# Optimization experiments

Measured on AMD Instinct MI355X. Metric: run time of the kernel, lower is better.

Reference implementation:

```python
import jax, jax.numpy as jnp
import numpy as np

NV, NC, NI = 20000, 300, 10000
NN = NV + NC + NI
E = 1_000_000
D = 64
HOPS = 2


def _segmax(src, idx, mask, n_seg):
    # scatter_max with torch_scatter semantics: empty segments -> 0
    idxm = jnp.where(mask, idx, n_seg)  # route masked edges to dump segment
    m = jax.ops.segment_max(src, idxm, num_segments=n_seg + 1)[:n_seg]
    return jnp.where(jnp.isfinite(m), m, 0.0)


def _segmin(src, idx, mask, n_seg):
    idxm = jnp.where(mask, idx, n_seg)
    m = jax.ops.segment_min(src, idxm, num_segments=n_seg + 1)[:n_seg]
    return jnp.where(jnp.isfinite(m), m, 0.0)


def _segmax_all(src, idx, n_seg):
    m = jax.ops.segment_max(src, idx, num_segments=n_seg)
    return jnp.where(jnp.isfinite(m), m, 0.0)


def _center(src, idx, mask, n_seg, W1, b1, W2, b2):
    # CenterIntersection: MLP -> scatter_softmax -> weighted scatter_sum
    idxm = jnp.where(mask, idx, n_seg)
    h = jax.nn.relu(src @ W1.T + b1)
    a = h @ W2.T + b2
    a = jnp.where(mask[:, None], a, 0.0)
    m = jax.ops.segment_max(a, idxm, num_segments=n_seg + 1)
    m = jnp.where(jnp.isfinite(m), m, 0.0)
    e = jnp.where(mask[:, None], jnp.exp(a - m[idxm]), 0.0)
    s = jax.ops.segment_sum(e, idxm, num_segments=n_seg + 1)
    att = e / jnp.where(s > 0, s, 1.0)[idxm]
    out = jax.ops.segment_sum(att * src, idxm, num_segments=n_seg + 1)
    return out[:n_seg]


def _l2norm(x, eps=1e-12):
    n = jnp.linalg.norm(x, axis=-1, keepdims=True)
    return x / jnp.maximum(n, eps)


def setup_inputs() -> dict:
    key = jax.random.key(0)
    ks = jax.random.split(key, 16)
    n = lambda k, s: jax.random.normal(k, s, dtype=jnp.float32)
    return dict(
        visit_emb=n(ks[0], (NV, D)), visit_offset=n(ks[1], (NV, D)),
        ccs_emb=n(ks[2], (NC, D)), ccs_offset=n(ks[3], (NC, D)),
        icd_emb=n(ks[4], (NI, D)), icd_offset=n(ks[5], (NI, D)),
        head=jax.random.randint(ks[6], (E,), 0, NN),
        tail=jax.random.randint(ks[7], (E,), 0, NN),
        visit_time=jax.random.uniform(ks[8], (NV,), minval=1.0, maxval=50.0, dtype=jnp.float32),
        cW1=n(ks[9], (D, D)) * 0.1, cb1=jnp.zeros((D,), jnp.float32),
        cW2=n(ks[10], (D, D)) * 0.1, cb2=jnp.zeros((D,), jnp.float32),
        tW1=n(ks[11], (1, 1)), tb1=jnp.zeros((1,), jnp.float32),
        tW2=n(ks[12], (1, 1)), tb2=jnp.zeros((1,), jnp.float32),
    )


def reference(visit_emb, visit_offset, ccs_emb, ccs_offset, icd_emb, icd_offset,
              head, tail, visit_time, cW1, cb1, cW2, cb2, tW1, tb1, tW2, tb2):
    all_embs = jnp.concatenate([visit_emb, ccs_emb, icd_emb], axis=0)          # [NN, D]
    all_off = jax.nn.relu(jnp.concatenate([visit_offset, ccs_offset, icd_offset], axis=0))

    # time attention: [NV, 1]
    t = (1.0 / visit_time)[:, None]
    l1 = jax.nn.relu(t @ tW1.T + tb1)
    time_emb = jax.nn.softmax(l1 @ tW2.T + tb2, axis=0)

    hv = head < NV
    uidx = jnp.tile(jnp.arange(NV), 3)

    for _ in range(HOPS):
        ev = hv & (tail >= NV)
        vv = hv & (tail < NV)
        # center aggregation: entity->visit hop, then time-weighted visit->visit hop
        hist = all_embs[tail]                                                  # [E, D]
        agg1 = _center(hist, head, ev, NN, cW1, cb1, cW2, cb2)
        agg2 = agg1[:NV] * time_emb
        hist2 = agg2[jnp.where(vv, tail, 0)]
        agg = _center(hist2, head, vv, NN, cW1, cb1, cW2, cb2)

        # box offset aggregation per edge type
        off_t = jax.nn.relu(all_off[tail])                                     # [E, D]
        iv = hv & (tail >= NV) & (tail < NV + NC)
        vi = hv & (tail >= NV + NC)
        iv_off = _segmax(off_t, head, iv, NN)[:NV]
        ut_off = _segmax(off_t, head, vi, NN)[:NV]
        vv_off = _segmax(off_t, head, vv, NN)[:NV]
        visit_off = jax.nn.relu(
            _segmax_all(jnp.concatenate([iv_off, ut_off, vv_off], axis=0), uidx, NV))
        cm = (head >= NV) & (head < NV + NC)
        ccs_off = _segmax(off_t, head, cm, NN)[NV:NV + NC]
        im = head >= NV + NC
        icd_off = _segmin(off_t, head, im, NN)[NV + NC:]

        all_embs = _l2norm(agg)
        all_off = jax.nn.relu(jnp.concatenate([visit_off, ccs_off, icd_off], axis=0))

    return all_embs[:NV], all_off[:NV]
```

## Files before the change

### kernel.cpp

```cpp
#include <hip/hip_runtime.h>

#define NV 20000
#define NC 300
#define NI 10000
#define NN 30300
#define NE 1000000
#define D  64

#define NB     128
#define BNODES 237
#define CAP    12288
#define BIN_CHUNK 2048
#define NBLK_BIN ((NE + BIN_CHUNK - 1) / BIN_CHUNK)

__device__ __forceinline__ unsigned short f2bf(float x) {
    unsigned u = __float_as_uint(x);
    u += 0x7FFFu + ((u >> 16) & 1u);
    return (unsigned short)(u >> 16);
}

__global__ void init_off_kernel(const float4* __restrict__ vo, const float4* __restrict__ co,
                                const float4* __restrict__ io, unsigned short* __restrict__ buf,
                                float4* __restrict__ outz) {
    int i = blockIdx.x * blockDim.x + threadIdx.x;
    if (i >= NN * 16) return;
    if (i < NV * 16) outz[i] = make_float4(0.f, 0.f, 0.f, 0.f);
    int n = i >> 4;
    float4 v;
    if (n < NV)            v = vo[i];
    else if (n < NV + NC)  v = co[i - NV * 16];
    else                   v = io[i - (NV + NC) * 16];
    ushort4 o;
    o.x = f2bf(fmaxf(v.x, 0.f));
    o.y = f2bf(fmaxf(v.y, 0.f));
    o.z = f2bf(fmaxf(v.z, 0.f));
    o.w = f2bf(fmaxf(v.w, 0.f));
    *reinterpret_cast<ushort4*>(buf + (size_t)i * 4) = o;
}

__global__ void bin_kernel(const int* __restrict__ head, const int* __restrict__ tail,
                           int* __restrict__ gcur, unsigned* __restrict__ pairs) {
    __shared__ int hist[NB];
    __shared__ int base[NB];
    int t = threadIdx.x;
    int e0 = blockIdx.x * BIN_CHUNK;
    if (t < NB) hist[t] = 0;
    __syncthreads();
    int hs[8], ts[8];
    if (e0 + BIN_CHUNK <= NE) {
        const int4* h4 = reinterpret_cast<const int4*>(head + e0);
        const int4* t4 = reinterpret_cast<const int4*>(tail + e0);
        int4 ha = h4[t], hb = h4[256 + t];
        int4 ta = t4[t], tb = t4[256 + t];
        hs[0] = ha.x; hs[1] = ha.y; hs[2] = ha.z; hs[3] = ha.w;
        hs[4] = hb.x; hs[5] = hb.y; hs[6] = hb.z; hs[7] = hb.w;
        ts[0] = ta.x; ts[1] = ta.y; ts[2] = ta.z; ts[3] = ta.w;
        ts[4] = tb.x; ts[5] = tb.y; ts[6] = tb.z; ts[7] = tb.w;
#pragma unroll
        for (int i = 0; i < 8; i++) atomicAdd(&hist[hs[i] / BNODES], 1);
    } else {
#pragma unroll
        for (int i = 0; i < 8; i++) {
            int e = e0 + i * 256 + t;
            if (e < NE) {
                hs[i] = head[e]; ts[i] = tail[e];
                atomicAdd(&hist[hs[i] / BNODES], 1);
            } else hs[i] = -1;
        }
    }
    __syncthreads();
    if (t < NB) {
        int c = hist[t];
        base[t] = c ? atomicAdd(&gcur[t], c) : 0;
        hist[t] = 0;
    }
    __syncthreads();
#pragma unroll
    for (int i = 0; i < 8; i++) {
        if (hs[i] >= 0) {
            int b = hs[i] / BNODES;
            int pos = base[b] + atomicAdd(&hist[b], 1);
            if (pos < CAP)
                pairs[(size_t)b * CAP + pos] = ((unsigned)hs[i] << 15) | (unsigned)ts[i];
        }
    }
}

__global__ void bucket_sort_kernel(const unsigned* __restrict__ pairs, const int* __restrict__ gcur,
                                   unsigned short* __restrict__ stails,
                                   int* __restrict__ starts, int* __restrict__ ends) {
    __shared__ unsigned short staging[CAP];
    __shared__ int cnt_l[256];
    __shared__ int scan_s[256];
    __shared__ int cur[256];
    int b = blockIdx.x, t = threadIdx.x;
    int node0 = b * BNODES;
    int nn = min(BNODES, NN - node0);
    int cnt = min(gcur[b], CAP);
    cnt_l[t] = 0;
    __syncthreads();
    const unsigned* P = pairs + (size_t)b * CAP;
    for (int i = t; i < cnt; i += 256) {
        int local = (int)(P[i] >> 15) - node0;
        atomicAdd(&cnt_l[local], 1);
    }
    __syncthreads();
    int v = cnt_l[t];
    scan_s[t] = v;
    __syncthreads();
    for (int off = 1; off < 256; off <<= 1) {
        int tv = (t >= off) ? scan_s[t - off] : 0;
        __syncthreads();
        scan_s[t] += tv;
        __syncthreads();
    }
    int excl = scan_s[t] - v;
    cur[t] = excl;
    if (t < nn) {
        starts[node0 + t] = b * CAP + excl;
        ends[node0 + t]   = b * CAP + excl + v;
    }
    __syncthreads();
    for (int i = t; i < cnt; i += 256) {
        unsigned p = P[i];
        int local = (int)(p >> 15) - node0;
        int pos = atomicAdd(&cur[local], 1);
        staging[pos] = (unsigned short)(p & 0x7FFFu);
    }
    __syncthreads();
    for (int i = t; i < cnt; i += 256)
        stails[(size_t)b * CAP + i] = staging[i];
}

template<bool F32OUT>
__global__ __launch_bounds__(256) void hop_kernel(
        const unsigned short* __restrict__ prev,
        const int* __restrict__ starts, const int* __restrict__ ends,
        const unsigned short* __restrict__ stails,
        void* __restrict__ outp, int nNodes) {
    int wid  = blockIdx.x * 4 + (threadIdx.x >> 6);
    int lane = threadIdx.x & 63;
    if (wid >= nNodes) return;
    int start = starts[wid], end = ends[wid];
    bool isMin = (!F32OUT) && (wid >= NV + NC);
    unsigned mm = isMin ? 0xFFFFFFFFu : 0u;
    int grp = lane >> 4, sub = lane & 15;
    const unsigned short* rowb = prev + sub * 4;
    unsigned a0 = 0, a1 = 0, a2 = 0, a3 = 0;
    int k = start;
    for (; k + 16 <= end; k += 16) {
#pragma unroll
        for (int r = 0; r < 4; ++r) {
            int tix = (int)stails[k + r * 4 + grp];
            uint2 v = *reinterpret_cast<const uint2*>(rowb + tix * D);
            v.x ^= mm; v.y ^= mm;
            a0 = max(a0, v.x & 0xFFFFu); a1 = max(a1, v.x >> 16);
            a2 = max(a2, v.y & 0xFFFFu); a3 = max(a3, v.y >> 16);
        }
    }
    for (; k < end; k += 4) {
        int e = k + grp;
        int tix = (int)stails[(e < end) ? e : (end - 1)];
        uint2 v = *reinterpret_cast<const uint2*>(rowb + tix * D);
        if (e >= end) { v.x = mm; v.y = mm; }
        v.x ^= mm; v.y ^= mm;
        a0 = max(a0, v.x & 0xFFFFu); a1 = max(a1, v.x >> 16);
        a2 = max(a2, v.y & 0xFFFFu); a3 = max(a3, v.y >> 16);
    }
    a0 = max(a0, (unsigned)__shfl_xor((int)a0, 16)); a0 = max(a0, (unsigned)__shfl_xor((int)a0, 32));
    a1 = max(a1, (unsigned)__shfl_xor((int)a1, 16)); a1 = max(a1, (unsigned)__shfl_xor((int)a1, 32));
    a2 = max(a2, (unsigned)__shfl_xor((int)a2, 16)); a2 = max(a2, (unsigned)__shfl_xor((int)a2, 32));
    a3 = max(a3, (unsigned)__shfl_xor((int)a3, 16)); a3 = max(a3, (unsigned)__shfl_xor((int)a3, 32));
    unsigned m16 = mm & 0xFFFFu;
    unsigned r0 = a0 ^ m16, r1 = a1 ^ m16, r2 = a2 ^ m16, r3 = a3 ^ m16;
    if (start >= end) { r0 = r1 = r2 = r3 = 0; }
    if (grp == 0) {
        if (F32OUT) {
            float4 o = make_float4(__uint_as_float(r0 << 16), __uint_as_float(r1 << 16),
                                   __uint_as_float(r2 << 16), __uint_as_float(r3 << 16));
            reinterpret_cast<float4*>(outp)[(size_t)wid * 16 + sub] = o;
        } else {
            ushort4 o;
            o.x = (unsigned short)r0; o.y = (unsigned short)r1;
            o.z = (unsigned short)r2; o.w = (unsigned short)r3;
            reinterpret_cast<ushort4*>(outp)[(size_t)wid * 16 + sub] = o;
        }
    }
}

extern "C" void kernel_launch(void* const* d_in, const int* in_sizes, int n_in,
                              void* d_out, int out_size, void* d_ws, size_t ws_size,
                              hipStream_t stream) {
    const float* visit_offset = (const float*)d_in[1];
    const float* ccs_offset   = (const float*)d_in[3];
    const float* icd_offset   = (const float*)d_in[5];
    const int*   head         = (const int*)d_in[6];
    const int*   tail         = (const int*)d_in[7];
    float*       out          = (float*)d_out;

    char* ws = (char*)d_ws;
    unsigned short* off0   = (unsigned short*)(ws);
    unsigned short* off1   = (unsigned short*)(ws + (4u << 20));
    unsigned*       pairs  = (unsigned*)      (ws + (8u << 20));
    unsigned short* stails = (unsigned short*)(ws + (14u << 20));
    int*            starts = (int*)           (ws + (17u << 20));
    int*            ends   = (int*)           (ws + (17u << 20) + (256u << 10));
    int*            gcur   = (int*)           (ws + (17u << 20) + (512u << 10));

    hipMemsetAsync(gcur, 0, NB * sizeof(int), stream);

    init_off_kernel<<<(NN * 16 + 255) / 256, 256, 0, stream>>>(
        (const float4*)visit_offset, (const float4*)ccs_offset, (const float4*)icd_offset,
        off0, (float4*)out);
    bin_kernel<<<NBLK_BIN, 256, 0, stream>>>(head, tail, gcur, pairs);
    bucket_sort_kernel<<<NB, 256, 0, stream>>>(pairs, gcur, stails, starts, ends);

    hop_kernel<false><<<(NN + 3) / 4, 256, 0, stream>>>(off0, starts, ends, stails, off1, NN);
    hop_kernel<true><<<(NV + 3) / 4, 256, 0, stream>>>(off1, starts, ends, stails,
                                                       out + (size_t)NV * D, NV);
}
```

Before: 163.6 us.

## Use finer node buckets, 16-byte gathers with shuffled tails, fold counter reset

Result: faster. 153.3 us (-6.3%).

```diff
diff --git a/kernel.cpp b/kernel.cpp
--- a/kernel.cpp
+++ b/kernel.cpp
@@ -7,9 +7,9 @@
 #define NE 1000000
 #define D  64
 
-#define NB     128
-#define BNODES 237
-#define CAP    12288
+#define NB     512
+#define BNODES 60
+#define CAP    2560
 #define BIN_CHUNK 2048
 #define NBLK_BIN ((NE + BIN_CHUNK - 1) / BIN_CHUNK)
 
@@ -21,8 +21,12 @@
 
 __global__ void init_off_kernel(const float4* __restrict__ vo, const float4* __restrict__ co,
                                 const float4* __restrict__ io, unsigned short* __restrict__ buf,
-                                float4* __restrict__ outz) {
+                                float4* __restrict__ outz, int* __restrict__ gcur) {
     int i = blockIdx.x * blockDim.x + threadIdx.x;
+    if (blockIdx.x == 0) {
+        gcur[threadIdx.x] = 0;
+        gcur[threadIdx.x + 256] = 0;
+    }
     if (i >= NN * 16) return;
     if (i < NV * 16) outz[i] = make_float4(0.f, 0.f, 0.f, 0.f);
     int n = i >> 4;
@@ -44,7 +48,7 @@
     __shared__ int base[NB];
     int t = threadIdx.x;
     int e0 = blockIdx.x * BIN_CHUNK;
-    if (t < NB) hist[t] = 0;
+    for (int j = t; j < NB; j += 256) hist[j] = 0;
     __syncthreads();
     int hs[8], ts[8];
     if (e0 + BIN_CHUNK <= NE) {
@@ -69,10 +73,10 @@
         }
     }
     __syncthreads();
-    if (t < NB) {
-        int c = hist[t];
-        base[t] = c ? atomicAdd(&gcur[t], c) : 0;
-        hist[t] = 0;
+    for (int j = t; j < NB; j += 256) {
+        int c = hist[j];
+        base[j] = c ? atomicAdd(&gcur[j], c) : 0;
+        hist[j] = 0;
     }
     __syncthreads();
 #pragma unroll
@@ -144,46 +148,58 @@
     int start = starts[wid], end = ends[wid];
     bool isMin = (!F32OUT) && (wid >= NV + NC);
     unsigned mm = isMin ? 0xFFFFFFFFu : 0u;
-    int grp = lane >> 4, sub = lane & 15;
-    const unsigned short* rowb = prev + sub * 4;
-    unsigned a0 = 0, a1 = 0, a2 = 0, a3 = 0;
-    int k = start;
-    for (; k + 16 <= end; k += 16) {
-#pragma unroll
-        for (int r = 0; r < 4; ++r) {
-            int tix = (int)stails[k + r * 4 + grp];
-            uint2 v = *reinterpret_cast<const uint2*>(rowb + tix * D);
-            v.x ^= mm; v.y ^= mm;
-            a0 = max(a0, v.x & 0xFFFFu); a1 = max(a1, v.x >> 16);
-            a2 = max(a2, v.y & 0xFFFFu); a3 = max(a3, v.y >> 16);
-        }
-    }
-    for (; k < end; k += 4) {
-        int e = k + grp;
-        int tix = (int)stails[(e < end) ? e : (end - 1)];
-        uint2 v = *reinterpret_cast<const uint2*>(rowb + tix * D);
-        if (e >= end) { v.x = mm; v.y = mm; }
-        v.x ^= mm; v.y ^= mm;
-        a0 = max(a0, v.x & 0xFFFFu); a1 = max(a1, v.x >> 16);
-        a2 = max(a2, v.y & 0xFFFFu); a3 = max(a3, v.y >> 16);
-    }
-    a0 = max(a0, (unsigned)__shfl_xor((int)a0, 16)); a0 = max(a0, (unsigned)__shfl_xor((int)a0, 32));
-    a1 = max(a1, (unsigned)__shfl_xor((int)a1, 16)); a1 = max(a1, (unsigned)__shfl_xor((int)a1, 32));
-    a2 = max(a2, (unsigned)__shfl_xor((int)a2, 16)); a2 = max(a2, (unsigned)__shfl_xor((int)a2, 32));
-    a3 = max(a3, (unsigned)__shfl_xor((int)a3, 16)); a3 = max(a3, (unsigned)__shfl_xor((int)a3, 32));
+    int grp = lane >> 3, sub = lane & 7;
+    const unsigned short* rowb = prev + sub * 8;
+    unsigned a0 = 0, a1 = 0, a2 = 0, a3 = 0,
+             a4 = 0, a5 = 0, a6 = 0, a7 = 0;
+    for (int base = start; base < end; base += 64) {
+        int cdeg = end - base; if (cdeg > 64) cdeg = 64;
+        int tv = (lane < cdeg) ? (int)stails[base + lane] : 0;
+        for (int r0 = 0; r0 < cdeg; r0 += 32) {
+#pragma unroll
+            for (int r = 0; r < 4; ++r) {
+                int e  = r0 + r * 8 + grp;
+                int ec = (e < cdeg) ? e : (cdeg - 1);
+                int tix = __shfl(tv, ec);
+                uint4 v = *reinterpret_cast<const uint4*>(rowb + tix * D);
+                unsigned live = (e < cdeg) ? 0xFFFFFFFFu : 0u;
+                v.x = (v.x ^ mm) & live; v.y = (v.y ^ mm) & live;
+                v.z = (v.z ^ mm) & live; v.w = (v.w ^ mm) & live;
+                a0 = max(a0, v.x & 0xFFFFu); a1 = max(a1, v.x >> 16);
+                a2 = max(a2, v.y & 0xFFFFu); a3 = max(a3, v.y >> 16);
+                a4 = max(a4, v.z & 0xFFFFu); a5 = max(a5, v.z >> 16);
+                a6 = max(a6, v.w & 0xFFFFu); a7 = max(a7, v.w >> 16);
+            }
+        }
+    }
+#pragma unroll
+    for (int d = 8; d < 64; d <<= 1) {
+        a0 = max(a0, (unsigned)__shfl_xor((int)a0, d));
+        a1 = max(a1, (unsigned)__shfl_xor((int)a1, d));
+        a2 = max(a2, (unsigned)__shfl_xor((int)a2, d));
+        a3 = max(a3, (unsigned)__shfl_xor((int)a3, d));
+        a4 = max(a4, (unsigned)__shfl_xor((int)a4, d));
+        a5 = max(a5, (unsigned)__shfl_xor((int)a5, d));
+        a6 = max(a6, (unsigned)__shfl_xor((int)a6, d));
+        a7 = max(a7, (unsigned)__shfl_xor((int)a7, d));
+    }
     unsigned m16 = mm & 0xFFFFu;
-    unsigned r0 = a0 ^ m16, r1 = a1 ^ m16, r2 = a2 ^ m16, r3 = a3 ^ m16;
-    if (start >= end) { r0 = r1 = r2 = r3 = 0; }
+    unsigned r0v = a0 ^ m16, r1v = a1 ^ m16, r2v = a2 ^ m16, r3v = a3 ^ m16;
+    unsigned r4v = a4 ^ m16, r5v = a5 ^ m16, r6v = a6 ^ m16, r7v = a7 ^ m16;
+    if (start >= end) { r0v=r1v=r2v=r3v=r4v=r5v=r6v=r7v=0; }
     if (grp == 0) {
         if (F32OUT) {
-            float4 o = make_float4(__uint_as_float(r0 << 16), __uint_as_float(r1 << 16),
-                                   __uint_as_float(r2 << 16), __uint_as_float(r3 << 16));
-            reinterpret_cast<float4*>(outp)[(size_t)wid * 16 + sub] = o;
+            float4 oa = make_float4(__uint_as_float(r0v << 16), __uint_as_float(r1v << 16),
+                                    __uint_as_float(r2v << 16), __uint_as_float(r3v << 16));
+            float4 ob = make_float4(__uint_as_float(r4v << 16), __uint_as_float(r5v << 16),
+                                    __uint_as_float(r6v << 16), __uint_as_float(r7v << 16));
+            float4* op = reinterpret_cast<float4*>(outp) + (size_t)wid * 16 + sub * 2;
+            op[0] = oa; op[1] = ob;
         } else {
-            ushort4 o;
-            o.x = (unsigned short)r0; o.y = (unsigned short)r1;
-            o.z = (unsigned short)r2; o.w = (unsigned short)r3;
-            reinterpret_cast<ushort4*>(outp)[(size_t)wid * 16 + sub] = o;
+            uint4 o;
+            o.x = r0v | (r1v << 16); o.y = r2v | (r3v << 16);
+            o.z = r4v | (r5v << 16); o.w = r6v | (r7v << 16);
+            reinterpret_cast<uint4*>(outp)[(size_t)wid * 8 + sub] = o;
         }
     }
 }
@@ -207,11 +223,9 @@
     int*            ends   = (int*)           (ws + (17u << 20) + (256u << 10));
     int*            gcur   = (int*)           (ws + (17u << 20) + (512u << 10));
 
-    hipMemsetAsync(gcur, 0, NB * sizeof(int), stream);
-
     init_off_kernel<<<(NN * 16 + 255) / 256, 256, 0, stream>>>(
         (const float4*)visit_offset, (const float4*)ccs_offset, (const float4*)icd_offset,
-        off0, (float4*)out);
+        off0, (float4*)out, gcur);
     bin_kernel<<<NBLK_BIN, 256, 0, stream>>>(head, tail, gcur, pairs);
     bucket_sort_kernel<<<NB, 256, 0, stream>>>(pairs, gcur, stails, starts, ends);
 
```
